# Kernel tuning notes

Hardware: AMD Instinct MI355X
Metric: run time of the kernel (lower is better)

## Reference

```python
import jax, jax.numpy as jnp
import numpy as np

N_QUBITS = 10
DIM = 2 ** N_QUBITS
N_POINTS = 64
D_FEAT = 10
N_LAYERS = 5

# bit tables: bits[:, q] = q-th least-significant bit of the state index.
# kron order in the original builds angles[n-1] x ... x angles[0], so angle q acts on bit q.
_bits = ((np.arange(DIM)[:, None] >> np.arange(N_QUBITS)[None, :]) & 1).astype(np.float32)
BITS_C = jnp.asarray(_bits - 0.5)  # (DIM, n): b_q - 1/2 -> rz diag phase coeffs
# crz ring: crz_matrix(i+1,...) is diagonal phase exp(i*theta*b_{i}*(b_{i+1}-1/2)) (control i, target i+1);
# close_ring is control n-1, target 0.
_ctrl = np.concatenate([np.arange(N_QUBITS - 1), [N_QUBITS - 1]])
_tgt = np.concatenate([np.arange(1, N_QUBITS), [0]])
RING_COEF = jnp.asarray(_bits[:, _ctrl] * (_bits[:, _tgt] - 0.5))  # (DIM, n)
H_GATES = jnp.broadcast_to(
    jnp.asarray((np.array([[1, 1], [1, -1]]) / np.sqrt(2)).astype(np.complex64)),
    (N_QUBITS, 2, 2))


def rz_diag(x, start):
    # rz_layer kron order: qubit q gets angle x[(start + n-1-q) % d]; rz = diag(e^{-it/2}, e^{it/2})
    idx = (start + N_QUBITS - 1 - np.arange(N_QUBITS)) % D_FEAT
    return jnp.exp(1j * (BITS_C @ x[idx]))  # (DIM,) complex64


def ring_diag(angles):
    return jnp.exp(1j * (RING_COEF @ angles))  # (DIM,) complex64


def ry_gates(angles):
    c, s = jnp.cos(0.5 * angles), jnp.sin(0.5 * angles)
    # (n, 2, 2): [[c, -s], [s, c]]
    return jnp.stack([jnp.stack([c, -s], -1), jnp.stack([s, c], -1)], -2).astype(jnp.complex64)


def apply_1q(state, gates):
    # apply gates[q] (2x2) to qubit q (axis n-1-q of the (2,)*n reshaped state)
    psi = state.reshape((2,) * N_QUBITS)
    for q in range(N_QUBITS):
        ax = N_QUBITS - 1 - q
        psi = jnp.moveaxis(jnp.tensordot(gates[q], psi, axes=([1], [ax])), 0, ax)
    return psi.reshape(DIM)


def block_f(state, x, bp, start):
    state = apply_1q(state, H_GATES)
    state = state * rz_diag(x, start)
    state = apply_1q(state, ry_gates(bp[0]))
    return state * ring_diag(bp[1])


def adj_block_f(state, x, bp, start):
    state = state * jnp.conj(ring_diag(bp[1]))
    state = apply_1q(state, ry_gates(-bp[0]))  # ry(t)^dagger = ry(-t)
    state = state * jnp.conj(rz_diag(x, start))
    return apply_1q(state, H_GATES)  # H is self-adjoint


def pair_prob(x1, x2, params):
    state = jnp.zeros((DIM,), jnp.complex64).at[0].set(1.0)
    for j in range(N_LAYERS):
        state = block_f(state, x1, params[j], j * N_QUBITS)
    for k in range(N_LAYERS):
        # faithful to original: start = (num_q - k - 1) * num_q (uses num_q, not n_layers)
        state = adj_block_f(state, x2, params[N_LAYERS - 1 - k], (N_QUBITS - k - 1) * N_QUBITS)
    a = state[0]
    return jnp.real(a) ** 2 + jnp.imag(a) ** 2  # |<0|U2^dag U1|0>|^2


def _kta(data, labels, params):
    x1 = jnp.repeat(data, N_POINTS, axis=0)   # point i of each pair
    x2 = jnp.tile(data, (N_POINTS, 1))        # point j of each pair
    k = jax.vmap(pair_prob, in_axes=(0, 0, None))(x1, x2, params)  # (N*N,)
    lm = (labels[:, None] * labels[None, :]).reshape(-1)
    kp = jnp.sum(lm * k)
    return kp / jnp.sqrt(jnp.sum(k * k) * jnp.sum(lm * lm))


def setup_inputs() -> dict:
    key = jax.random.key(0)
    k1, k2, k3 = jax.random.split(key, 3)
    data = jax.random.normal(k1, (N_POINTS, D_FEAT), jnp.float32)
    labels = jnp.where(jax.random.normal(k2, (N_POINTS,)) >= 0, 1.0, -1.0).astype(jnp.float32)
    params = jax.random.uniform(k3, (N_LAYERS, 2, N_QUBITS), jnp.float32, 0.0, 2.0 * np.pi)
    return {"data": data, "labels": labels, "params": params}


def reference(data, labels, params):
    return _kta(data, labels, params)
```

## Files before the change

kernel.cpp:

```cpp
#include <hip/hip_runtime.h>
#include <math.h>

#define NQ 10
#define DIM 1024
#define NPTS 64
#define DFEAT 10
#define NLAYERS 5
#define NPAIR 2080
#define GBLK  (NPAIR / 4)

#define IS2 0.70710678118654752440f

#define PART_OFF ((size_t)NPTS * DIM * sizeof(float2))

__global__ __launch_bounds__(1024) void state_kernel(
    const float* __restrict__ data,
    const float* __restrict__ params,
    float2* __restrict__ psi)
{
    const int i    = blockIdx.x;
    const int tid  = threadIdx.x;
    const int lane = tid & 63;

    __shared__ float4 mc[NLAYERS][NQ];
    __shared__ float2 xbuf[DIM];

    if (tid < NLAYERS * NQ) {
        const int L = tid / NQ, q = tid - L * NQ;
        const float xh = 0.5f * data[i * DFEAT + (9 - q)];
        const float cx = __cosf(xh), sx = __sinf(xh);
        float c = 1.f, s = 0.f;
        if (L != NLAYERS - 1) {
            const float th = 0.5f * params[L * 2 * NQ + q];
            c = __cosf(th); s = __sinf(th);
        }
        const float p = (c + s) * IS2, qm = (c - s) * IS2;
        mc[L][q] = make_float4(qm * cx, -p * sx, p * cx, -qm * sx);
    }
    __syncthreads();

    float re, im;
    {
        float Pr = 1.f, Pi = 0.f;
#pragma unroll 1
        for (int q = 0; q < NQ; ++q) {
            const float4 m = mc[0][q];
            const int b = (tid >> q) & 1;
            const float fr = b ? m.z : m.x;
            const float fi = b ? -m.w : m.y;
            const float nr = Pr * fr - Pi * fi;
            const float ni = Pr * fi + Pi * fr;
            Pr = nr; Pi = ni;
        }
        re = Pr; im = Pi;
    }

#pragma unroll 1
    for (int L = 0; L < NLAYERS; ++L) {
        if (L > 0) {
#pragma unroll 1
            for (int q = 0; q < 6; ++q) {
                const float4 m = mc[L][q];
                const int   b = (lane >> q) & 1;
                const float msr = b ? -m.x : m.x;
                const float msi = m.y;
                const float mpr = m.z;
                const float mpi = b ? -m.w : m.w;
                const float pr = __shfl_xor(re, 1 << q, 64);
                const float pi = __shfl_xor(im, 1 << q, 64);
                const float nr = msr * re - msi * im + mpr * pr - mpi * pi;
                const float ni = msr * im + msi * re + mpr * pi + mpi * pr;
                re = nr; im = ni;
            }
#pragma unroll 1
            for (int q = 6; q < NQ; ++q) {
                const float4 m = mc[L][q];
                const int   b = (tid >> q) & 1;
                const float msr = b ? -m.x : m.x;
                const float msi = m.y;
                const float mpr = m.z;
                const float mpi = b ? -m.w : m.w;
                xbuf[tid] = make_float2(re, im);
                __syncthreads();
                const float2 p2 = xbuf[tid ^ (1 << q)];
                const float nr = msr * re - msi * im + mpr * p2.x - mpi * p2.y;
                const float ni = msr * im + msi * re + mpr * p2.y + mpi * p2.x;
                re = nr; im = ni;
                __syncthreads();
            }
        }

        if (L < NLAYERS - 1) {
            const float* rg = params + L * 2 * NQ + NQ;
            float ph = 0.f;
#pragma unroll 1
            for (int n = 0; n < NQ; ++n) {
                const int   nn = (n == 9) ? 0 : (n + 1);
                const float g  = rg[n];
                const float t  = (((tid >> nn) & 1) ? 0.5f : -0.5f) * g;
                ph += ((tid >> n) & 1) ? t : 0.f;
            }
            const float s = __sinf(ph), c = __cosf(ph);
            const float nr = re * c - im * s;
            const float ni = re * s + im * c;
            re = nr; im = ni;
        }
    }

    psi[i * DIM + tid] = make_float2(re, im);
}

__global__ __launch_bounds__(256) void gram_kernel(
    const float4* __restrict__ psi4,
    const float* __restrict__ labels,
    float* __restrict__ partials)
{
    __shared__ float sm[2][4];
    const int wave = threadIdx.x >> 6;
    const int lane = threadIdx.x & 63;
    const int w    = blockIdx.x * 4 + wave;

    int i = (int)((129.0f - sqrtf(16641.0f - 8.0f * (float)w)) * 0.5f);
    int Ci = 64 * i - ((i * (i - 1)) >> 1);
    while (w < Ci)            { --i; Ci = 64 * i - ((i * (i - 1)) >> 1); }
    while (w >= Ci + 64 - i)  { Ci += 64 - i; ++i; }
    const int j = i + (w - Ci);

    const float4* a = psi4 + i * (DIM / 2);
    const float4* b = psi4 + j * (DIM / 2);

    float zr = 0.f, zi = 0.f;
#pragma unroll
    for (int r = 0; r < 8; ++r) {
        const int k = (r << 6) | lane;
        const float4 av = a[k], bv = b[k];
        zr += bv.x * av.x + bv.y * av.y + bv.z * av.z + bv.w * av.w;
        zi += bv.x * av.y - bv.y * av.x + bv.z * av.w - bv.w * av.z;
    }
#pragma unroll
    for (int off = 32; off; off >>= 1) {
        zr += __shfl_xor(zr, off, 64);
        zi += __shfl_xor(zi, off, 64);
    }

    if (lane == 0) {
        const float k = zr * zr + zi * zi;
        const float wgt = (i == j) ? 1.f : 2.f;
        sm[0][wave] = wgt * labels[i] * labels[j] * k;
        sm[1][wave] = wgt * k * k;
    }
    __syncthreads();
    if (threadIdx.x == 0) {
        partials[2 * blockIdx.x]     = sm[0][0] + sm[0][1] + sm[0][2] + sm[0][3];
        partials[2 * blockIdx.x + 1] = sm[1][0] + sm[1][1] + sm[1][2] + sm[1][3];
    }
}

__global__ __launch_bounds__(256) void reduce_kernel(
    const float* __restrict__ partials,
    const float* __restrict__ labels,
    float* __restrict__ out)
{
    __shared__ float sm[3][4];
    const int tid  = threadIdx.x;
    const int lane = tid & 63;
    const int wave = tid >> 6;

    float slk = 0.f, skk = 0.f, sl2 = 0.f;
    for (int p = tid; p < GBLK; p += 256) {
        slk += partials[2 * p];
        skk += partials[2 * p + 1];
    }
    if (tid < NPTS) { const float l = labels[tid]; sl2 = l * l; }

#pragma unroll
    for (int off = 32; off; off >>= 1) {
        slk += __shfl_xor(slk, off, 64);
        skk += __shfl_xor(skk, off, 64);
        sl2 += __shfl_xor(sl2, off, 64);
    }
    if (lane == 0) { sm[0][wave] = slk; sm[1][wave] = skk; sm[2][wave] = sl2; }
    __syncthreads();
    if (tid == 0) {
        const float a = sm[0][0] + sm[0][1] + sm[0][2] + sm[0][3];
        const float b = sm[1][0] + sm[1][1] + sm[1][2] + sm[1][3];
        const float c = sm[2][0] + sm[2][1] + sm[2][2] + sm[2][3];
        out[0] = a / sqrtf(b * (c * c));
    }
}

extern "C" void kernel_launch(void* const* d_in, const int* in_sizes, int n_in,
                              void* d_out, int out_size, void* d_ws, size_t ws_size,
                              hipStream_t stream) {
    const float* data   = (const float*)d_in[0];
    const float* labels = (const float*)d_in[1];
    const float* params = (const float*)d_in[2];
    float* out = (float*)d_out;

    float2* psi      = (float2*)d_ws;
    float*  partials = (float*)((char*)d_ws + PART_OFF);

    state_kernel <<<NPTS, 1024, 0, stream>>>(data, params, psi);
    gram_kernel  <<<GBLK,  256, 0, stream>>>((const float4*)psi, labels, partials);
    reduce_kernel<<<1,     256, 0, stream>>>(partials, labels, out);
}
```

Measured before the change: 73.89 us.

## Fuse final reduction into gram kernel via atomics and double-buffer state exchange

Removes the separate reduce kernel launch. The gram kernel now uses 64 blocks that loop over pairs, accumulate into 16 atomic buckets, and let the last-arriving block (tracked by a ticket counter) compute the final ratio. The state kernel zeroes the accumulators and double-buffers its shared exchange array, which drops one __syncthreads per high-qubit gate. The trade-offs are fewer gram blocks, which means less parallelism for the memory reads, plus atomic contention and a reliance on ordering between kernels.

Result: slower. 84.20 us (+13.9%).

```diff
diff --git a/kernel.cpp b/kernel.cpp
--- a/kernel.cpp
+++ b/kernel.cpp
@@ -7,23 +7,26 @@
 #define DFEAT 10
 #define NLAYERS 5
 #define NPAIR 2080
-#define GBLK  (NPAIR / 4)
+#define NBUCKET 16
 
 #define IS2 0.70710678118654752440f
 
-#define PART_OFF ((size_t)NPTS * DIM * sizeof(float2))
+#define ACC_OFF ((size_t)NPTS * DIM * sizeof(float2))
 
 __global__ __launch_bounds__(1024) void state_kernel(
     const float* __restrict__ data,
     const float* __restrict__ params,
-    float2* __restrict__ psi)
+    float2* __restrict__ psi,
+    float* __restrict__ acc)
 {
     const int i    = blockIdx.x;
     const int tid  = threadIdx.x;
     const int lane = tid & 63;
 
+    if (i == 0 && tid < 2 * NBUCKET + 1) acc[tid] = 0.f;
+
     __shared__ float4 mc[NLAYERS][NQ];
-    __shared__ float2 xbuf[DIM];
+    __shared__ float2 xb[2][DIM];
 
     if (tid < NLAYERS * NQ) {
         const int L = tid / NQ, q = tid - L * NQ;
@@ -54,6 +57,8 @@
         }
         re = Pr; im = Pi;
     }
+
+    int sp = 0;
 
 #pragma unroll 1
     for (int L = 0; L < NLAYERS; ++L) {
@@ -80,13 +85,13 @@
                 const float msi = m.y;
                 const float mpr = m.z;
                 const float mpi = b ? -m.w : m.w;
-                xbuf[tid] = make_float2(re, im);
+                xb[sp][tid] = make_float2(re, im);
                 __syncthreads();
-                const float2 p2 = xbuf[tid ^ (1 << q)];
+                const float2 p2 = xb[sp][tid ^ (1 << q)];
                 const float nr = msr * re - msi * im + mpr * p2.x - mpi * p2.y;
                 const float ni = msr * im + msi * re + mpr * p2.y + mpi * p2.x;
                 re = nr; im = ni;
-                __syncthreads();
+                sp ^= 1;
             }
         }
 
@@ -113,79 +118,74 @@
 __global__ __launch_bounds__(256) void gram_kernel(
     const float4* __restrict__ psi4,
     const float* __restrict__ labels,
-    float* __restrict__ partials)
+    float* __restrict__ acc,
+    float* __restrict__ out)
 {
     __shared__ float sm[2][4];
-    const int wave = threadIdx.x >> 6;
-    const int lane = threadIdx.x & 63;
-    const int w    = blockIdx.x * 4 + wave;
-
-    int i = (int)((129.0f - sqrtf(16641.0f - 8.0f * (float)w)) * 0.5f);
-    int Ci = 64 * i - ((i * (i - 1)) >> 1);
-    while (w < Ci)            { --i; Ci = 64 * i - ((i * (i - 1)) >> 1); }
-    while (w >= Ci + 64 - i)  { Ci += 64 - i; ++i; }
-    const int j = i + (w - Ci);
-
-    const float4* a = psi4 + i * (DIM / 2);
-    const float4* b = psi4 + j * (DIM / 2);
-
-    float zr = 0.f, zi = 0.f;
+    __shared__ int   islast;
+    const int blk  = blockIdx.x;
+    const int tid  = threadIdx.x;
+    const int wv   = tid >> 6;
+    const int lane = tid & 63;
+    const int g    = blk * 4 + wv;
+
+    float wslk = 0.f, wskk = 0.f;
+#pragma unroll 1
+    for (int w = g; w < NPAIR; w += 256) {
+        int i = (int)((129.0f - sqrtf(16641.0f - 8.0f * (float)w)) * 0.5f);
+        int Ci = 64 * i - ((i * (i - 1)) >> 1);
+        while (w < Ci)            { --i; Ci = 64 * i - ((i * (i - 1)) >> 1); }
+        while (w >= Ci + 64 - i)  { Ci += 64 - i; ++i; }
+        const int j = i + (w - Ci);
+
+        const float4* a = psi4 + i * (DIM / 2);
+        const float4* b = psi4 + j * (DIM / 2);
+        float zr = 0.f, zi = 0.f;
 #pragma unroll
-    for (int r = 0; r < 8; ++r) {
-        const int k = (r << 6) | lane;
-        const float4 av = a[k], bv = b[k];
-        zr += bv.x * av.x + bv.y * av.y + bv.z * av.z + bv.w * av.w;
-        zi += bv.x * av.y - bv.y * av.x + bv.z * av.w - bv.w * av.z;
-    }
+        for (int r = 0; r < 8; ++r) {
+            const int k = (r << 6) | lane;
+            const float4 av = a[k], bv = b[k];
+            zr += bv.x * av.x + bv.y * av.y + bv.z * av.z + bv.w * av.w;
+            zi += bv.x * av.y - bv.y * av.x + bv.z * av.w - bv.w * av.z;
+        }
 #pragma unroll
-    for (int off = 32; off; off >>= 1) {
-        zr += __shfl_xor(zr, off, 64);
-        zi += __shfl_xor(zi, off, 64);
-    }
-
-    if (lane == 0) {
-        const float k = zr * zr + zi * zi;
+        for (int off = 32; off; off >>= 1) {
+            zr += __shfl_xor(zr, off, 64);
+            zi += __shfl_xor(zi, off, 64);
+        }
+        const float k   = zr * zr + zi * zi;
         const float wgt = (i == j) ? 1.f : 2.f;
-        sm[0][wave] = wgt * labels[i] * labels[j] * k;
-        sm[1][wave] = wgt * k * k;
-    }
+        wslk += wgt * labels[i] * labels[j] * k;
+        wskk += wgt * k * k;
+    }
+
+    if (lane == 0) { sm[0][wv] = wslk; sm[1][wv] = wskk; }
     __syncthreads();
-    if (threadIdx.x == 0) {
-        partials[2 * blockIdx.x]     = sm[0][0] + sm[0][1] + sm[0][2] + sm[0][3];
-        partials[2 * blockIdx.x + 1] = sm[1][0] + sm[1][1] + sm[1][2] + sm[1][3];
-    }
-}
-
-__global__ __launch_bounds__(256) void reduce_kernel(
-    const float* __restrict__ partials,
-    const float* __restrict__ labels,
-    float* __restrict__ out)
-{
-    __shared__ float sm[3][4];
-    const int tid  = threadIdx.x;
-    const int lane = tid & 63;
-    const int wave = tid >> 6;
-
-    float slk = 0.f, skk = 0.f, sl2 = 0.f;
-    for (int p = tid; p < GBLK; p += 256) {
-        slk += partials[2 * p];
-        skk += partials[2 * p + 1];
-    }
-    if (tid < NPTS) { const float l = labels[tid]; sl2 = l * l; }
-
+
+    if (tid == 0) {
+        const float bs = sm[0][0] + sm[0][1] + sm[0][2] + sm[0][3];
+        const float bk = sm[1][0] + sm[1][1] + sm[1][2] + sm[1][3];
+        const int bkt = blk & (NBUCKET - 1);
+        atomicAdd(&acc[bkt], bs);
+        atomicAdd(&acc[NBUCKET + bkt], bk);
+        __threadfence();
+        unsigned* ticket = (unsigned*)(acc + 2 * NBUCKET);
+        islast = (atomicAdd(ticket, 1u) == (unsigned)(gridDim.x - 1)) ? 1 : 0;
+    }
+    __syncthreads();
+
+    if (islast && wv == 0) {
+        float va = (lane < NBUCKET) ? atomicAdd(&acc[lane], 0.f) : 0.f;
+        float vb = (lane < NBUCKET) ? atomicAdd(&acc[NBUCKET + lane], 0.f) : 0.f;
+        const float l = labels[lane];
+        float vl = l * l;
 #pragma unroll
-    for (int off = 32; off; off >>= 1) {
-        slk += __shfl_xor(slk, off, 64);
-        skk += __shfl_xor(skk, off, 64);
-        sl2 += __shfl_xor(sl2, off, 64);
-    }
-    if (lane == 0) { sm[0][wave] = slk; sm[1][wave] = skk; sm[2][wave] = sl2; }
-    __syncthreads();
-    if (tid == 0) {
-        const float a = sm[0][0] + sm[0][1] + sm[0][2] + sm[0][3];
-        const float b = sm[1][0] + sm[1][1] + sm[1][2] + sm[1][3];
-        const float c = sm[2][0] + sm[2][1] + sm[2][2] + sm[2][3];
-        out[0] = a / sqrtf(b * (c * c));
+        for (int off = 32; off; off >>= 1) {
+            va += __shfl_xor(va, off, 64);
+            vb += __shfl_xor(vb, off, 64);
+            vl += __shfl_xor(vl, off, 64);
+        }
+        if (lane == 0) out[0] = va / sqrtf(vb * (vl * vl));
     }
 }
 
@@ -197,10 +197,9 @@
     const float* params = (const float*)d_in[2];
     float* out = (float*)d_out;
 
-    float2* psi      = (float2*)d_ws;
-    float*  partials = (float*)((char*)d_ws + PART_OFF);
-
-    state_kernel <<<NPTS, 1024, 0, stream>>>(data, params, psi);
-    gram_kernel  <<<GBLK,  256, 0, stream>>>((const float4*)psi, labels, partials);
-    reduce_kernel<<<1,     256, 0, stream>>>(partials, labels, out);
+    float2* psi = (float2*)d_ws;
+    float*  acc = (float*)((char*)d_ws + ACC_OFF);
+
+    state_kernel<<<NPTS, 1024, 0, stream>>>(data, params, psi, acc);
+    gram_kernel <<<NPTS,  256, 0, stream>>>((const float4*)psi, labels, acc, out);
 }
```
